# Performance work log

Measured on AMD Instinct MI355X. Metric: run time of the kernel, lower is better.

## Reference

```python
import jax, jax.numpy as jnp
import numpy as np

B, S, D, H = 4, 2048, 1024, 16
DH = D // H  # 64


def setup_inputs() -> dict:
    key = jax.random.key(0)
    ks = jax.random.split(key, 7)
    scale = 1.0 / np.sqrt(DH)
    return {
        "sequences": jax.random.normal(ks[0], (B, S, D), dtype=jnp.float32),
        # torch Linear weights: [out, in] per head -> stacked [H, DH, DH]
        "Wq": jax.random.uniform(ks[1], (H, DH, DH), jnp.float32, -scale, scale),
        "bq": jax.random.uniform(ks[2], (H, DH), jnp.float32, -scale, scale),
        "Wk": jax.random.uniform(ks[3], (H, DH, DH), jnp.float32, -scale, scale),
        "bk": jax.random.uniform(ks[4], (H, DH), jnp.float32, -scale, scale),
        "Wv": jax.random.uniform(ks[5], (H, DH, DH), jnp.float32, -scale, scale),
        "bv": jax.random.uniform(ks[6], (H, DH), jnp.float32, -scale, scale),
    }


def reference(sequences, Wq, bq, Wk, bk, Wv, bv):
    # split d into heads: [B, S, H, DH]
    x = sequences.reshape(B, S, H, DH)
    # per-head Linear: y = x @ W.T + b
    q = jnp.einsum("bshd,hed->bshe", x, Wq) + bq
    k = jnp.einsum("bshd,hed->bshe", x, Wk) + bk
    v = jnp.einsum("bshd,hed->bshe", x, Wv) + bv
    # scaled dot-product attention per head
    scores = jnp.einsum("bshd,bthd->bhst", q, k) / jnp.sqrt(jnp.float32(DH))
    attn = jax.nn.softmax(scores, axis=-1)
    out = jnp.einsum("bhst,bthd->bshd", attn, v)
    # hstack heads back to [B, S, D]
    return out.reshape(B, S, D)
```

## Files before the change

### kernel.cpp

```cpp
#include <hip/hip_runtime.h>
#include <hip/hip_bf16.h>


typedef unsigned short u16;
typedef unsigned int   u32;
typedef float  f32x4  __attribute__((ext_vector_type(4)));
typedef __bf16 bf16x4 __attribute__((ext_vector_type(4)));
typedef __bf16 bf16x8 __attribute__((ext_vector_type(8)));

#define NB 4
#define SS 2048
#define DDIM 1024
#define NH 16
#define DH 64

static __device__ __forceinline__ float fexp2(float x) {
#if __has_builtin(__builtin_amdgcn_exp2f)
    return __builtin_amdgcn_exp2f(x);
#else
    return exp2f(x);
#endif
}
static __device__ __forceinline__ bf16x4 cvt4(f32x4 v) {
    return __builtin_convertvector(v, bf16x4);
}
static __device__ __forceinline__ bf16x8 cvt8(f32x4 lo, f32x4 hi) {
    return __builtin_shufflevector(cvt4(lo), cvt4(hi), 0, 1, 2, 3, 4, 5, 6, 7);
}

#define WST 72

__global__ __launch_bounds__(256) void qkv_kernel(
        const float* __restrict__ x,
        const float* __restrict__ Wq, const float* __restrict__ bq,
        const float* __restrict__ Wk, const float* __restrict__ bk,
        const float* __restrict__ Wv, const float* __restrict__ bv,
        u16* __restrict__ Qw, u16* __restrict__ Kw, u16* __restrict__ Vt) {
    __shared__ __align__(16) u16 W_lds[3 * DH * WST];

    const int tid  = threadIdx.x;
    const int w    = tid >> 6;
    const int lane = tid & 63;
    const int quad = lane >> 4;
    const int c    = lane & 15;
    const int bid  = blockIdx.x;
    const int bh   = bid & 63;
    const int s0   = (bid >> 6) * 128;
    const int b    = bh >> 4, h = bh & 15;

    {
        const float* Wsrc[3] = {Wq + h*DH*DH, Wk + h*DH*DH, Wv + h*DH*DH};
        #pragma unroll
        for (int j = 0; j < 6; ++j) {
            const int m = j >> 1;
            const int chunk = ((j & 1) << 8) + tid;
            const float* src = Wsrc[m] + chunk * 8;
            f32x4 lo = *(const f32x4*)src;
            f32x4 hi = *(const f32x4*)(src + 4);
            const int row = chunk >> 3, c8 = chunk & 7;
            *(bf16x8*)&W_lds[(m*DH + row) * WST + c8*8] = cvt8(lo, hi);
        }
    }

    const int sbA = s0 + w*32;
    const int sbB = sbA + 16;
    const float* xrA = x + ((size_t)(b * SS + sbA + c)) * DDIM + h * DH;
    const float* xrB = x + ((size_t)(b * SS + sbB + c)) * DDIM + h * DH;
    f32x4 a0 = *(const f32x4*)(xrA + quad*8);
    f32x4 a1 = *(const f32x4*)(xrA + quad*8 + 4);
    f32x4 a2 = *(const f32x4*)(xrA + 32 + quad*8);
    f32x4 a3 = *(const f32x4*)(xrA + 32 + quad*8 + 4);
    f32x4 b0 = *(const f32x4*)(xrB + quad*8);
    f32x4 b1 = *(const f32x4*)(xrB + quad*8 + 4);
    f32x4 b2 = *(const f32x4*)(xrB + 32 + quad*8);
    f32x4 b3 = *(const f32x4*)(xrB + 32 + quad*8 + 4);

    f32x4 biasQK[2][4];
    float biasV[4];
    #pragma unroll
    for (int mt = 0; mt < 4; ++mt) {
        biasQK[0][mt] = *(const f32x4*)(bq + h*DH + mt*16 + quad*4);
        biasQK[1][mt] = *(const f32x4*)(bk + h*DH + mt*16 + quad*4);
        biasV[mt] = bv[h*DH + mt*16 + c];
    }

    __syncthreads();

    bf16x8 xbA[2] = { cvt8(a0, a1), cvt8(a2, a3) };
    bf16x8 xbB[2] = { cvt8(b0, b1), cvt8(b2, b3) };

    const size_t qkbase = (size_t)bh * SS * DH;
    const size_t vtbase = (size_t)bh * DH * SS;

    const int srowA = sbA + c, srowB = sbB + c;
    const int tqA = srowA & 31, tqB = srowB & 31;
    const int sKA = (srowA & ~31) | ((tqA & 4) << 2) | ((tqA >> 3) << 2) | (tqA & 3);
    const int sKB = (srowB & ~31) | ((tqB & 4) << 2) | ((tqB >> 3) << 2) | (tqB & 3);

    #pragma unroll
    for (int m = 0; m < 2; ++m) {
        const float scale = (m == 0) ? 0.18033688f : 1.0f;
        u16* baseA = (m == 0 ? Qw : Kw) + qkbase + (size_t)(m == 0 ? srowA : sKA) * DH;
        u16* baseB = (m == 0 ? Qw : Kw) + qkbase + (size_t)(m == 0 ? srowB : sKB) * DH;
        #pragma unroll
        for (int mt = 0; mt < 4; ++mt) {
            const bf16x8 w0 = *(const bf16x8*)&W_lds[(m*DH + mt*16 + c) * WST + quad*8];
            const bf16x8 w1 = *(const bf16x8*)&W_lds[(m*DH + mt*16 + c) * WST + 32 + quad*8];
            f32x4 accA = {0.f, 0.f, 0.f, 0.f};
            accA = __builtin_amdgcn_mfma_f32_16x16x32_bf16(w0, xbA[0], accA, 0, 0, 0);
            accA = __builtin_amdgcn_mfma_f32_16x16x32_bf16(w1, xbA[1], accA, 0, 0, 0);
            f32x4 accB = {0.f, 0.f, 0.f, 0.f};
            accB = __builtin_amdgcn_mfma_f32_16x16x32_bf16(w0, xbB[0], accB, 0, 0, 0);
            accB = __builtin_amdgcn_mfma_f32_16x16x32_bf16(w1, xbB[1], accB, 0, 0, 0);
            f32x4 vA = (accA + biasQK[m][mt]) * scale;
            f32x4 vB = (accB + biasQK[m][mt]) * scale;
            *(bf16x4*)(baseA + mt*16 + quad*4) = cvt4(vA);
            *(bf16x4*)(baseB + mt*16 + quad*4) = cvt4(vB);
        }
    }
    #pragma unroll
    for (int nt = 0; nt < 4; ++nt) {
        const bf16x8 w0 = *(const bf16x8*)&W_lds[(2*DH + nt*16 + c) * WST + quad*8];
        const bf16x8 w1 = *(const bf16x8*)&W_lds[(2*DH + nt*16 + c) * WST + 32 + quad*8];
        f32x4 accA = {0.f, 0.f, 0.f, 0.f};
        accA = __builtin_amdgcn_mfma_f32_16x16x32_bf16(xbA[0], w0, accA, 0, 0, 0);
        accA = __builtin_amdgcn_mfma_f32_16x16x32_bf16(xbA[1], w1, accA, 0, 0, 0);
        f32x4 accB = {0.f, 0.f, 0.f, 0.f};
        accB = __builtin_amdgcn_mfma_f32_16x16x32_bf16(xbB[0], w0, accB, 0, 0, 0);
        accB = __builtin_amdgcn_mfma_f32_16x16x32_bf16(xbB[1], w1, accB, 0, 0, 0);
        f32x4 vA = accA + biasV[nt];
        f32x4 vB = accB + biasV[nt];
        u16* dstA = Vt + vtbase + (size_t)(nt*16 + c) * SS + sbA + quad*4;
        u16* dstB = Vt + vtbase + (size_t)(nt*16 + c) * SS + sbB + quad*4;
        *(bf16x4*)dstA = cvt4(vA);
        *(bf16x4*)dstB = cvt4(vB);
    }
}

#define KT 128
#define KST 72
#define VST 136

#define LOAD_FRAGS(kf, vf, g) do {                                             \
        kf[0] = *(const bf16x8*)&Kl[((g)*32 + c) * KST + quad*8];              \
        kf[1] = *(const bf16x8*)&Kl[((g)*32 + c) * KST + 32 + quad*8];         \
        kf[2] = *(const bf16x8*)&Kl[((g)*32 + 16 + c) * KST + quad*8];         \
        kf[3] = *(const bf16x8*)&Kl[((g)*32 + 16 + c) * KST + 32 + quad*8];    \
        vf[0] = *(const bf16x8*)&Vl[( 0 + c) * VST + (g)*32 + quad*8];         \
        vf[1] = *(const bf16x8*)&Vl[(16 + c) * VST + (g)*32 + quad*8];         \
        vf[2] = *(const bf16x8*)&Vl[(32 + c) * VST + (g)*32 + quad*8];         \
        vf[3] = *(const bf16x8*)&Vl[(48 + c) * VST + (g)*32 + quad*8];         \
    } while (0)

#define COMPUTE_G(kf, vf) do {                                                 \
        __builtin_amdgcn_s_setprio(1);                                         \
        _Pragma("unroll")                                                      \
        for (int qt = 0; qt < 4; ++qt) {                                       \
            f32x4 sA = {0.f,0.f,0.f,0.f}, sB = {0.f,0.f,0.f,0.f};              \
            sA = __builtin_amdgcn_mfma_f32_16x16x32_bf16(kf[0], qf[qt][0], sA, 0,0,0); \
            sA = __builtin_amdgcn_mfma_f32_16x16x32_bf16(kf[1], qf[qt][1], sA, 0,0,0); \
            sB = __builtin_amdgcn_mfma_f32_16x16x32_bf16(kf[2], qf[qt][0], sB, 0,0,0); \
            sB = __builtin_amdgcn_mfma_f32_16x16x32_bf16(kf[3], qf[qt][1], sB, 0,0,0); \
            f32x4 eA, eB;                                                      \
            _Pragma("unroll")                                                  \
            for (int r = 0; r < 4; ++r) { eA[r] = fexp2(sA[r]); eB[r] = fexp2(sB[r]); } \
            bf16x8 pf = cvt8(eA, eB);                                          \
            o[0][qt] = __builtin_amdgcn_mfma_f32_16x16x32_bf16(vf[0], pf, o[0][qt], 0,0,0); \
            o[1][qt] = __builtin_amdgcn_mfma_f32_16x16x32_bf16(vf[1], pf, o[1][qt], 0,0,0); \
            o[2][qt] = __builtin_amdgcn_mfma_f32_16x16x32_bf16(vf[2], pf, o[2][qt], 0,0,0); \
            o[3][qt] = __builtin_amdgcn_mfma_f32_16x16x32_bf16(vf[3], pf, o[3][qt], 0,0,0); \
            lacc[qt] = __builtin_amdgcn_mfma_f32_16x16x32_bf16(ones8, pf, lacc[qt], 0,0,0); \
        }                                                                      \
        __builtin_amdgcn_s_setprio(0);                                         \
    } while (0)

__global__ __launch_bounds__(256, 2) void attn_kernel(
        const u16* __restrict__ Qw, const u16* __restrict__ Kw,
        const u16* __restrict__ Vt, float* __restrict__ out) {
    __shared__ __align__(16) u16 K_lds[2][KT * KST];
    __shared__ __align__(16) u16 V_lds[2][DH * VST];

    const int tid  = threadIdx.x;
    const int w    = tid >> 6;
    const int lane = tid & 63;
    const int quad = lane >> 4;
    const int c    = lane & 15;
    const int bid  = blockIdx.x;
    const int bh   = bid & 63;
    const int q0   = (bid >> 6) * 256;
    const int qw   = q0 + w * 64;

    const u16* Qb = Qw + (size_t)bh * SS * DH;
    const u16* Kb = Kw + (size_t)bh * SS * DH;
    const u16* Vb = Vt + (size_t)bh * DH * SS;

    bf16x8 qf[4][2];
    #pragma unroll
    for (int qt = 0; qt < 4; ++qt) {
        const u16* qrow = Qb + (size_t)(qw + qt*16 + c) * DH;
        qf[qt][0] = *(const bf16x8*)(qrow + quad*8);
        qf[qt][1] = *(const bf16x8*)(qrow + 32 + quad*8);
    }

    f32x4 o[4][4];
    f32x4 lacc[4];
    #pragma unroll
    for (int qt = 0; qt < 4; ++qt) {
        lacc[qt] = (f32x4){0.f, 0.f, 0.f, 0.f};
        #pragma unroll
        for (int dt = 0; dt < 4; ++dt) o[dt][qt] = (f32x4){0.f, 0.f, 0.f, 0.f};
    }

    bf16x8 ones8;
    { union { u16 u[8]; bf16x8 v; } one;
      #pragma unroll
      for (int i = 0; i < 8; ++i) one.u[i] = 0x3F80;
      ones8 = one.v; }

    const int krow = tid >> 1;
    const int kcol = (tid & 1) * 32;
    const int kofs = krow * KST + kcol;
    const int vrow = tid >> 2;
    const int vcol = (tid & 3) * 32;
    const int vofs = vrow * VST + vcol;

    uint4 kr0 = *(const uint4*)(Kb + (size_t)krow * DH + kcol);
    uint4 kr1 = *(const uint4*)(Kb + (size_t)krow * DH + kcol + 8);
    uint4 kr2 = *(const uint4*)(Kb + (size_t)krow * DH + kcol + 16);
    uint4 kr3 = *(const uint4*)(Kb + (size_t)krow * DH + kcol + 24);
    uint4 vr0 = *(const uint4*)(Vb + (size_t)vrow * SS + vcol);
    uint4 vr1 = *(const uint4*)(Vb + (size_t)vrow * SS + vcol + 8);
    uint4 vr2 = *(const uint4*)(Vb + (size_t)vrow * SS + vcol + 16);
    uint4 vr3 = *(const uint4*)(Vb + (size_t)vrow * SS + vcol + 24);

    #pragma unroll 1
    for (int t0 = 0; t0 < SS; t0 += KT) {
        const int bsel = (t0 >> 7) & 1;
        u16* Kl = K_lds[bsel];
        u16* Vl = V_lds[bsel];
        *(uint4*)&Kl[kofs]      = kr0;
        *(uint4*)&Kl[kofs + 8]  = kr1;
        *(uint4*)&Kl[kofs + 16] = kr2;
        *(uint4*)&Kl[kofs + 24] = kr3;
        *(uint4*)&Vl[vofs]      = vr0;
        *(uint4*)&Vl[vofs + 8]  = vr1;
        *(uint4*)&Vl[vofs + 16] = vr2;
        *(uint4*)&Vl[vofs + 24] = vr3;
        __syncthreads();
        int tn = t0 + KT; if (tn >= SS) tn = 0;
        kr0 = *(const uint4*)(Kb + (size_t)(tn + krow) * DH + kcol);
        kr1 = *(const uint4*)(Kb + (size_t)(tn + krow) * DH + kcol + 8);
        kr2 = *(const uint4*)(Kb + (size_t)(tn + krow) * DH + kcol + 16);
        kr3 = *(const uint4*)(Kb + (size_t)(tn + krow) * DH + kcol + 24);
        vr0 = *(const uint4*)(Vb + (size_t)vrow * SS + tn + vcol);
        vr1 = *(const uint4*)(Vb + (size_t)vrow * SS + tn + vcol + 8);
        vr2 = *(const uint4*)(Vb + (size_t)vrow * SS + tn + vcol + 16);
        vr3 = *(const uint4*)(Vb + (size_t)vrow * SS + tn + vcol + 24);

        bf16x8 kfA[4], vfA[4], kfB[4], vfB[4];
        LOAD_FRAGS(kfA, vfA, 0);
        LOAD_FRAGS(kfB, vfB, 1);
        COMPUTE_G(kfA, vfA);
        LOAD_FRAGS(kfA, vfA, 2);
        COMPUTE_G(kfB, vfB);
        LOAD_FRAGS(kfB, vfB, 3);
        COMPUTE_G(kfA, vfA);
        COMPUTE_G(kfB, vfB);
    }

    const int b = bh >> 4, h = bh & 15;
    #pragma unroll
    for (int qt = 0; qt < 4; ++qt) {
        const float inv = 1.0f / lacc[qt][0];
        const int token = qw + qt*16 + c;
        float* orow = out + ((size_t)b * SS + token) * DDIM + h * DH;
        #pragma unroll
        for (int dt = 0; dt < 4; ++dt) {
            f32x4 vv = o[dt][qt] * inv;
            *(f32x4*)(orow + dt*16 + quad*4) = vv;
        }
    }
}

extern "C" void kernel_launch(void* const* d_in, const int* in_sizes, int n_in,
                              void* d_out, int out_size, void* d_ws, size_t ws_size,
                              hipStream_t stream) {
    const float* x  = (const float*)d_in[0];
    const float* Wq = (const float*)d_in[1];
    const float* bq = (const float*)d_in[2];
    const float* Wk = (const float*)d_in[3];
    const float* bk = (const float*)d_in[4];
    const float* Wv = (const float*)d_in[5];
    const float* bv = (const float*)d_in[6];

    u16* Qw = (u16*)d_ws;
    u16* Kw = Qw + (size_t)NB * NH * SS * DH;
    u16* Vt = Kw + (size_t)NB * NH * SS * DH;

    qkv_kernel<<<64 * (SS / 128), 256, 0, stream>>>(
        x, Wq, bq, Wk, bk, Wv, bv, Qw, Kw, Vt);
    attn_kernel<<<64 * (SS / 256), 256, 0, stream>>>(Qw, Kw, Vt, (float*)d_out);
}
```

Before: 169.7 us.

## Give each wave a private K/V LDS tile to eliminate block barriers

Replaces the block-shared, double-buffered 128-key K/V tiles with per-wave 32-key tiles that each wave loads and reads itself, removing __syncthreads from the main loop. This is meant to remove barrier stalls between waves. In exchange, every wave fetches K and V from global memory independently, so global/L2 traffic is multiplied by four. The loop also runs more iterations with less work per iteration to hide latency.

```diff
diff --git a/kernel.cpp b/kernel.cpp
--- a/kernel.cpp
+++ b/kernel.cpp
@@ -137,48 +137,15 @@
     }
 }
 
-#define KT 128
+#define KT 32
 #define KST 72
-#define VST 136
-
-#define LOAD_FRAGS(kf, vf, g) do {                                             \
-        kf[0] = *(const bf16x8*)&Kl[((g)*32 + c) * KST + quad*8];              \
-        kf[1] = *(const bf16x8*)&Kl[((g)*32 + c) * KST + 32 + quad*8];         \
-        kf[2] = *(const bf16x8*)&Kl[((g)*32 + 16 + c) * KST + quad*8];         \
-        kf[3] = *(const bf16x8*)&Kl[((g)*32 + 16 + c) * KST + 32 + quad*8];    \
-        vf[0] = *(const bf16x8*)&Vl[( 0 + c) * VST + (g)*32 + quad*8];         \
-        vf[1] = *(const bf16x8*)&Vl[(16 + c) * VST + (g)*32 + quad*8];         \
-        vf[2] = *(const bf16x8*)&Vl[(32 + c) * VST + (g)*32 + quad*8];         \
-        vf[3] = *(const bf16x8*)&Vl[(48 + c) * VST + (g)*32 + quad*8];         \
-    } while (0)
-
-#define COMPUTE_G(kf, vf) do {                                                 \
-        __builtin_amdgcn_s_setprio(1);                                         \
-        _Pragma("unroll")                                                      \
-        for (int qt = 0; qt < 4; ++qt) {                                       \
-            f32x4 sA = {0.f,0.f,0.f,0.f}, sB = {0.f,0.f,0.f,0.f};              \
-            sA = __builtin_amdgcn_mfma_f32_16x16x32_bf16(kf[0], qf[qt][0], sA, 0,0,0); \
-            sA = __builtin_amdgcn_mfma_f32_16x16x32_bf16(kf[1], qf[qt][1], sA, 0,0,0); \
-            sB = __builtin_amdgcn_mfma_f32_16x16x32_bf16(kf[2], qf[qt][0], sB, 0,0,0); \
-            sB = __builtin_amdgcn_mfma_f32_16x16x32_bf16(kf[3], qf[qt][1], sB, 0,0,0); \
-            f32x4 eA, eB;                                                      \
-            _Pragma("unroll")                                                  \
-            for (int r = 0; r < 4; ++r) { eA[r] = fexp2(sA[r]); eB[r] = fexp2(sB[r]); } \
-            bf16x8 pf = cvt8(eA, eB);                                          \
-            o[0][qt] = __builtin_amdgcn_mfma_f32_16x16x32_bf16(vf[0], pf, o[0][qt], 0,0,0); \
-            o[1][qt] = __builtin_amdgcn_mfma_f32_16x16x32_bf16(vf[1], pf, o[1][qt], 0,0,0); \
-            o[2][qt] = __builtin_amdgcn_mfma_f32_16x16x32_bf16(vf[2], pf, o[2][qt], 0,0,0); \
-            o[3][qt] = __builtin_amdgcn_mfma_f32_16x16x32_bf16(vf[3], pf, o[3][qt], 0,0,0); \
-            lacc[qt] = __builtin_amdgcn_mfma_f32_16x16x32_bf16(ones8, pf, lacc[qt], 0,0,0); \
-        }                                                                      \
-        __builtin_amdgcn_s_setprio(0);                                         \
-    } while (0)
+#define VST 40
+#define WKV (32*KST + 64*VST)
 
 __global__ __launch_bounds__(256, 2) void attn_kernel(
         const u16* __restrict__ Qw, const u16* __restrict__ Kw,
         const u16* __restrict__ Vt, float* __restrict__ out) {
-    __shared__ __align__(16) u16 K_lds[2][KT * KST];
-    __shared__ __align__(16) u16 V_lds[2][DH * VST];
+    __shared__ __align__(16) u16 lds[4 * WKV];
 
     const int tid  = threadIdx.x;
     const int w    = tid >> 6;
@@ -194,6 +161,9 @@
     const u16* Kb = Kw + (size_t)bh * SS * DH;
     const u16* Vb = Vt + (size_t)bh * DH * SS;
 
+    u16* wK = lds + w * WKV;
+    u16* wV = wK + 32 * KST;
+
     bf16x8 qf[4][2];
     #pragma unroll
     for (int qt = 0; qt < 4; ++qt) {
@@ -217,55 +187,69 @@
       for (int i = 0; i < 8; ++i) one.u[i] = 0x3F80;
       ones8 = one.v; }
 
-    const int krow = tid >> 1;
-    const int kcol = (tid & 1) * 32;
-    const int kofs = krow * KST + kcol;
-    const int vrow = tid >> 2;
-    const int vcol = (tid & 3) * 32;
-    const int vofs = vrow * VST + vcol;
-
-    uint4 kr0 = *(const uint4*)(Kb + (size_t)krow * DH + kcol);
-    uint4 kr1 = *(const uint4*)(Kb + (size_t)krow * DH + kcol + 8);
-    uint4 kr2 = *(const uint4*)(Kb + (size_t)krow * DH + kcol + 16);
-    uint4 kr3 = *(const uint4*)(Kb + (size_t)krow * DH + kcol + 24);
-    uint4 vr0 = *(const uint4*)(Vb + (size_t)vrow * SS + vcol);
-    uint4 vr1 = *(const uint4*)(Vb + (size_t)vrow * SS + vcol + 8);
-    uint4 vr2 = *(const uint4*)(Vb + (size_t)vrow * SS + vcol + 16);
-    uint4 vr3 = *(const uint4*)(Vb + (size_t)vrow * SS + vcol + 24);
+    const int klr = lane >> 1;
+    const int klc = (lane & 1) * 32;
+    const int vlr = lane >> 2;
+    const int vlc = (lane & 3) * 8;
+
+    uint4 kr0 = *(const uint4*)(Kb + (size_t)klr * DH + klc);
+    uint4 kr1 = *(const uint4*)(Kb + (size_t)klr * DH + klc + 8);
+    uint4 kr2 = *(const uint4*)(Kb + (size_t)klr * DH + klc + 16);
+    uint4 kr3 = *(const uint4*)(Kb + (size_t)klr * DH + klc + 24);
+    uint4 vr0 = *(const uint4*)(Vb + (size_t)( 0 + vlr) * SS + vlc);
+    uint4 vr1 = *(const uint4*)(Vb + (size_t)(16 + vlr) * SS + vlc);
+    uint4 vr2 = *(const uint4*)(Vb + (size_t)(32 + vlr) * SS + vlc);
+    uint4 vr3 = *(const uint4*)(Vb + (size_t)(48 + vlr) * SS + vlc);
 
     #pragma unroll 1
     for (int t0 = 0; t0 < SS; t0 += KT) {
-        const int bsel = (t0 >> 7) & 1;
-        u16* Kl = K_lds[bsel];
-        u16* Vl = V_lds[bsel];
-        *(uint4*)&Kl[kofs]      = kr0;
-        *(uint4*)&Kl[kofs + 8]  = kr1;
-        *(uint4*)&Kl[kofs + 16] = kr2;
-        *(uint4*)&Kl[kofs + 24] = kr3;
-        *(uint4*)&Vl[vofs]      = vr0;
-        *(uint4*)&Vl[vofs + 8]  = vr1;
-        *(uint4*)&Vl[vofs + 16] = vr2;
-        *(uint4*)&Vl[vofs + 24] = vr3;
-        __syncthreads();
+        *(uint4*)&wK[klr*KST + klc]      = kr0;
+        *(uint4*)&wK[klr*KST + klc + 8]  = kr1;
+        *(uint4*)&wK[klr*KST + klc + 16] = kr2;
+        *(uint4*)&wK[klr*KST + klc + 24] = kr3;
+        *(uint4*)&wV[( 0 + vlr)*VST + vlc] = vr0;
+        *(uint4*)&wV[(16 + vlr)*VST + vlc] = vr1;
+        *(uint4*)&wV[(32 + vlr)*VST + vlc] = vr2;
+        *(uint4*)&wV[(48 + vlr)*VST + vlc] = vr3;
+
         int tn = t0 + KT; if (tn >= SS) tn = 0;
-        kr0 = *(const uint4*)(Kb + (size_t)(tn + krow) * DH + kcol);
-        kr1 = *(const uint4*)(Kb + (size_t)(tn + krow) * DH + kcol + 8);
-        kr2 = *(const uint4*)(Kb + (size_t)(tn + krow) * DH + kcol + 16);
-        kr3 = *(const uint4*)(Kb + (size_t)(tn + krow) * DH + kcol + 24);
-        vr0 = *(const uint4*)(Vb + (size_t)vrow * SS + tn + vcol);
-        vr1 = *(const uint4*)(Vb + (size_t)vrow * SS + tn + vcol + 8);
-        vr2 = *(const uint4*)(Vb + (size_t)vrow * SS + tn + vcol + 16);
-        vr3 = *(const uint4*)(Vb + (size_t)vrow * SS + tn + vcol + 24);
-
-        bf16x8 kfA[4], vfA[4], kfB[4], vfB[4];
-        LOAD_FRAGS(kfA, vfA, 0);
-        LOAD_FRAGS(kfB, vfB, 1);
-        COMPUTE_G(kfA, vfA);
-        LOAD_FRAGS(kfA, vfA, 2);
-        COMPUTE_G(kfB, vfB);
-        LOAD_FRAGS(kfB, vfB, 3);
-        COMPUTE_G(kfA, vfA);
-        COMPUTE_G(kfB, vfB);
+        kr0 = *(const uint4*)(Kb + (size_t)(tn + klr) * DH + klc);
+        kr1 = *(const uint4*)(Kb + (size_t)(tn + klr) * DH + klc + 8);
+        kr2 = *(const uint4*)(Kb + (size_t)(tn + klr) * DH + klc + 16);
+        kr3 = *(const uint4*)(Kb + (size_t)(tn + klr) * DH + klc + 24);
+        vr0 = *(const uint4*)(Vb + (size_t)( 0 + vlr) * SS + tn + vlc);
+        vr1 = *(const uint4*)(Vb + (size_t)(16 + vlr) * SS + tn + vlc);
+        vr2 = *(const uint4*)(Vb + (size_t)(32 + vlr) * SS + tn + vlc);
+        vr3 = *(const uint4*)(Vb + (size_t)(48 + vlr) * SS + tn + vlc);
+
+        bf16x8 kf0 = *(const bf16x8*)&wK[(     c)*KST +      quad*8];
+        bf16x8 kf1 = *(const bf16x8*)&wK[(     c)*KST + 32 + quad*8];
+        bf16x8 kf2 = *(const bf16x8*)&wK[(16 + c)*KST +      quad*8];
+        bf16x8 kf3 = *(const bf16x8*)&wK[(16 + c)*KST + 32 + quad*8];
+        bf16x8 vf0 = *(const bf16x8*)&wV[(     c)*VST + quad*8];
+        bf16x8 vf1 = *(const bf16x8*)&wV[(16 + c)*VST + quad*8];
+        bf16x8 vf2 = *(const bf16x8*)&wV[(32 + c)*VST + quad*8];
+        bf16x8 vf3 = *(const bf16x8*)&wV[(48 + c)*VST + quad*8];
+
+        __builtin_amdgcn_s_setprio(1);
+        #pragma unroll
+        for (int qt = 0; qt < 4; ++qt) {
+            f32x4 sA = {0.f,0.f,0.f,0.f}, sB = {0.f,0.f,0.f,0.f};
+            sA = __builtin_amdgcn_mfma_f32_16x16x32_bf16(kf0, qf[qt][0], sA, 0,0,0);
+            sA = __builtin_amdgcn_mfma_f32_16x16x32_bf16(kf1, qf[qt][1], sA, 0,0,0);
+            sB = __builtin_amdgcn_mfma_f32_16x16x32_bf16(kf2, qf[qt][0], sB, 0,0,0);
+            sB = __builtin_amdgcn_mfma_f32_16x16x32_bf16(kf3, qf[qt][1], sB, 0,0,0);
+            f32x4 eA, eB;
+            #pragma unroll
+            for (int r = 0; r < 4; ++r) { eA[r] = fexp2(sA[r]); eB[r] = fexp2(sB[r]); }
+            bf16x8 pf = cvt8(eA, eB);
+            o[0][qt] = __builtin_amdgcn_mfma_f32_16x16x32_bf16(vf0, pf, o[0][qt], 0,0,0);
+            o[1][qt] = __builtin_amdgcn_mfma_f32_16x16x32_bf16(vf1, pf, o[1][qt], 0,0,0);
+            o[2][qt] = __builtin_amdgcn_mfma_f32_16x16x32_bf16(vf2, pf, o[2][qt], 0,0,0);
+            o[3][qt] = __builtin_amdgcn_mfma_f32_16x16x32_bf16(vf3, pf, o[3][qt], 0,0,0);
+            lacc[qt] = __builtin_amdgcn_mfma_f32_16x16x32_bf16(ones8, pf, lacc[qt], 0,0,0);
+        }
+        __builtin_amdgcn_s_setprio(0);
     }
 
     const int b = bh >> 4, h = bh & 15;
```

New measurement: 179.3 us. 5.7% more time.
